# Kernel optimization log

Measured on AMD Instinct MI355X. Metric: run time of the kernel, lower is better.

## Reference

```python
import jax, jax.numpy as jnp
import numpy as np

C = 64
CK = C // 8  # query/key channels


def setup_inputs() -> dict:
    key = jax.random.key(0)
    ks = jax.random.split(key, 8)
    b, c, h, w = 4, C, 64, 64
    x = jax.random.normal(ks[0], (b, c, h, w), dtype=jnp.float32)
    # 1x1 conv weights (spectral-normalized weights are still just dense weights at eval)
    wq = jax.random.normal(ks[1], (CK, c), dtype=jnp.float32) * 0.05
    bq = jax.random.normal(ks[2], (CK,), dtype=jnp.float32) * 0.01
    wk = jax.random.normal(ks[3], (CK, c), dtype=jnp.float32) * 0.05
    bk = jax.random.normal(ks[4], (CK,), dtype=jnp.float32) * 0.01
    wv = jax.random.normal(ks[5], (c, c), dtype=jnp.float32) * 0.05
    bv = jax.random.normal(ks[6], (c,), dtype=jnp.float32) * 0.01
    # gamma is initialized to 0 in the module; use a nonzero value so the
    # attention path contributes to the output.
    gamma = jax.random.normal(ks[7], (1,), dtype=jnp.float32) * 0.5
    return {"x": x, "wq": wq, "bq": bq, "wk": wk, "bk": bk,
            "wv": wv, "bv": bv, "gamma": gamma}


def reference(x, wq, bq, wk, bk, wv, bv, gamma):
    b, c, h, w = x.shape
    n = h * w
    xf = x.reshape(b, c, n)                      # [b, c, n]
    # 1x1 convs as matmuls over the channel dim
    q = jnp.einsum('oc,bcn->bno', wq, xf) + bq   # [b, n, ck]
    k = jnp.einsum('oc,bcn->bon', wk, xf) + bk[None, :, None]  # [b, ck, n]
    v = jnp.einsum('oc,bcn->bno', wv, xf) + bv   # [b, n, c]
    attn = jax.nn.softmax(jnp.einsum('bnd,bdm->bnm', q, k), axis=-1)  # [b, n, n]
    o = jnp.einsum('bnm,bmc->bnc', attn, v)      # [b, n, c]
    o = o.transpose(0, 2, 1).reshape(b, c, h, w)
    return gamma[0] * o + x
```

## Files before the change

### kernel.cpp

```cpp
#include <hip/hip_runtime.h>

#define CH 64
#define NN 4096
#define NB 4
#define SPLIT 8
#define KLEN (NN / SPLIT)
#define KTILE 128
#define NT (KLEN / KTILE)
#define QBLK 256
#define LOG2E 1.44269504f

typedef unsigned short u16;
typedef unsigned int u32;
typedef __attribute__((ext_vector_type(8))) short bf16x8;
typedef __attribute__((ext_vector_type(16))) float f32x16;

static __device__ __forceinline__ u16 bf16r(float f) {
  union { float f; unsigned u; } v; v.f = f;
  unsigned x = v.u;
  x += 0x7fffu + ((x >> 16) & 1u);
  return (u16)(x >> 16);
}
static __device__ __forceinline__ u32 pk2(float a, float b) {
  union { float f; unsigned u; } va, vb; va.f = a; vb.f = b;
  unsigned x = va.u, y = vb.u;
  x += 0x7fffu + ((x >> 16) & 1u);
  y += 0x7fffu + ((y >> 16) & 1u);
  return (x >> 16) | (y & 0xffff0000u);
}

__global__ __launch_bounds__(128) void qkv_proj(
    const float* __restrict__ x,
    const float* __restrict__ wq, const float* __restrict__ bq,
    const float* __restrict__ wk, const float* __restrict__ bk,
    const float* __restrict__ wv, const float* __restrict__ bv,
    u16* __restrict__ Qb, u16* __restrict__ Kb, u16* __restrict__ Vb) {
  __shared__ u16 afr_lds[3][4][64][8];
  __shared__ float bvs[64];
  const int tid = threadIdx.x;

  for (int idx = tid; idx < 3 * 4 * 64; idx += 128) {
    const int l = idx & 63;
    const int s = (idx >> 6) & 3;
    const int t = idx >> 8;
    const int row = 32 * t + (l & 31);
    const int c0 = 16 * s + 8 * (l >> 5);
    float e[8];
#pragma unroll
    for (int j = 0; j < 8; ++j) {
      float v = 0.f;
      if (row < 64)      v = wv[row * 64 + c0 + j];
      else if (row < 72) v = wq[(row - 64) * 64 + c0 + j];
      else if (row < 80) v = wk[(row - 72) * 64 + c0 + j];
      e[j] = v;
    }
    u32* dst = reinterpret_cast<u32*>(&afr_lds[t][s][l][0]);
    dst[0] = pk2(e[0], e[1]); dst[1] = pk2(e[2], e[3]);
    dst[2] = pk2(e[4], e[5]); dst[3] = pk2(e[6], e[7]);
  }
  if (tid < 64) bvs[tid] = bv[tid];
  __syncthreads();

  const int b = blockIdx.x >> 6;
  const int n0 = (blockIdx.x & 63) << 6;
  const int w = tid >> 6;
  const int lane = tid & 63;
  const int l31 = lane & 31;
  const int h = lane >> 5;
  const int n = n0 + 32 * w + l31;

  bf16x8 afr[3][4];
#pragma unroll
  for (int t = 0; t < 3; ++t)
#pragma unroll
    for (int s = 0; s < 4; ++s)
      afr[t][s] = *reinterpret_cast<const bf16x8*>(&afr_lds[t][s][lane][0]);

  f32x16 acc[3] = {{}, {}, {}};
  const float* xb = x + (size_t)b * CH * NN + n;
#pragma unroll
  for (int s = 0; s < 4; ++s) {
    float xv[8];
#pragma unroll
    for (int j = 0; j < 8; ++j)
      xv[j] = xb[(size_t)(16 * s + 8 * h + j) * NN];
    union { uint4 u; bf16x8 v; } bf;
    bf.u.x = pk2(xv[0], xv[1]); bf.u.y = pk2(xv[2], xv[3]);
    bf.u.z = pk2(xv[4], xv[5]); bf.u.w = pk2(xv[6], xv[7]);
#pragma unroll
    for (int t = 0; t < 3; ++t)
      acc[t] = __builtin_amdgcn_mfma_f32_32x32x16_bf16(afr[t][s], bf.v, acc[t], 0, 0, 0);
  }

  const int sperm = (l31 & 19) | ((l31 & 4) << 1) | ((l31 & 8) >> 1);
  const int nperm = n0 + 32 * w + sperm;
#pragma unroll
  for (int t = 0; t < 2; ++t)
#pragma unroll
    for (int r = 0; r < 16; ++r) {
      const int row = 32 * t + (r & 3) + 8 * (r >> 2) + 4 * h;
      Vb[((size_t)b * CH + row) * NN + nperm] = bf16r(acc[t][r] + bvs[row]);
    }
#pragma unroll
  for (int r = 0; r < 8; ++r) {
    const int row = (r & 3) + 8 * (r >> 2) + 4 * h;
    const float v = acc[2][r];
    if (row < 8)
      Qb[((size_t)b * NN + n) * 8 + row] = bf16r((v + bq[row]) * LOG2E);
    else
      Kb[((size_t)b * NN + n) * 8 + (row - 8)] = bf16r(v + bk[row - 8]);
  }
}

__global__ __launch_bounds__(512, 4) void flash_attn(
    const u16* __restrict__ Qb, const u16* __restrict__ Kb,
    const u16* __restrict__ Vb, u32* __restrict__ ACCu,
    float* __restrict__ Lb) {
  __shared__ u16 Klds[2][1032];
  __shared__ u16 Vlds[2][8192];
  const int bid = blockIdx.x;
  const int sp = bid & 7;
  const int rest = bid >> 3;
  const int qb = rest & 15;
  const int b = rest >> 4;
  const int w = __builtin_amdgcn_readfirstlane(threadIdx.x >> 6);
  const int lane = threadIdx.x & 63;
  const int l31 = lane & 31;
  const int h = lane >> 5;
  const int x7 = l31 & 7;
  const int qrow0 = qb * QBLK + w * 32;
  const int ks = sp * KLEN;

  if (threadIdx.x < 8) {
    Klds[0][1024 + threadIdx.x] = 0;
    Klds[1][1024 + threadIdx.x] = 0;
  }

  bf16x8 qf = {0, 0, 0, 0, 0, 0, 0, 0};
  if (h == 0)
    qf = *reinterpret_cast<const bf16x8*>(Qb + ((size_t)b * NN + qrow0 + l31) * 8);

  const u16* Kp = Kb + ((size_t)b * NN + ks) * 8;
  const u16* Vp = Vb + (size_t)b * CH * NN + ks;

  const int c15 = lane & 15;
  const int vr0 = w * 8 + (lane >> 4);
  const int vr1 = vr0 + 4;
  const size_t vsrc0 = (size_t)vr0 * NN + (size_t)(((c15 & 8) | ((c15 ^ vr0) & 7)) * 8);
  const size_t vsrc1 = (size_t)vr1 * NN + (size_t)(((c15 & 8) | ((c15 ^ vr1) & 7)) * 8);

#define STAGE(tt, bb) do {                                                    \
    __builtin_amdgcn_global_load_lds(                                         \
        (const __attribute__((address_space(1))) void*)(Vp + vsrc0 + (tt) * KTILE), \
        (__attribute__((address_space(3))) void*)&Vlds[bb][(w * 8) * 128], 16, 0, 0); \
    __builtin_amdgcn_global_load_lds(                                         \
        (const __attribute__((address_space(1))) void*)(Vp + vsrc1 + (tt) * KTILE), \
        (__attribute__((address_space(3))) void*)&Vlds[bb][(w * 8 + 4) * 128], 16, 0, 0); \
    if (w < 2)                                                                \
      __builtin_amdgcn_global_load_lds(                                       \
          (const __attribute__((address_space(1))) void*)(Kp + ((size_t)(tt) * KTILE + w * 64 + lane) * 8), \
          (__attribute__((address_space(3))) void*)&Klds[bb][w * 512], 16, 0, 0); \
  } while (0)

  f32x16 acc0 = {}, acc1 = {};
  const f32x16 zz = {};
  float lsum = 0.f;

  STAGE(0, 0);
#pragma unroll
  for (int t = 0; t < NT; ++t) {
    const int buf = t & 1;
    __syncthreads();
    if (t + 1 < NT) STAGE(t + 1, buf ^ 1);
    const u16* Kl = &Klds[buf][0];
    const u16* Vl = &Vlds[buf][0];
#pragma unroll
    for (int k32 = 0; k32 < 4; ++k32) {
      const int kaddr = h ? 1024 : (k32 * 32 + l31) * 8;
      bf16x8 kf = *reinterpret_cast<const bf16x8*>(Kl + kaddr);
      f32x16 s = __builtin_amdgcn_mfma_f32_32x32x16_bf16(kf, qf, zz, 0, 0, 0);
      float p[16];
#pragma unroll
      for (int r = 0; r < 16; ++r) { p[r] = exp2f(s[r]); lsum += p[r]; }
      union { uint4 u; bf16x8 v; } pb0, pb1;
      pb0.u.x = pk2(p[0], p[1]);   pb0.u.y = pk2(p[2], p[3]);
      pb0.u.z = pk2(p[4], p[5]);   pb0.u.w = pk2(p[6], p[7]);
      pb1.u.x = pk2(p[8], p[9]);   pb1.u.y = pk2(p[10], p[11]);
      pb1.u.z = pk2(p[12], p[13]); pb1.u.w = pk2(p[14], p[15]);
      const int c16_0 = k32 * 4 + h;
      const int c16_1 = c16_0 + 2;
      const int cp0 = (c16_0 & 8) | ((c16_0 ^ x7) & 7);
      const int cp1 = (c16_1 & 8) | ((c16_1 ^ x7) & 7);
      bf16x8 v00 = *reinterpret_cast<const bf16x8*>(Vl + l31 * 128 + cp0 * 8);
      bf16x8 v01 = *reinterpret_cast<const bf16x8*>(Vl + l31 * 128 + cp1 * 8);
      bf16x8 v10 = *reinterpret_cast<const bf16x8*>(Vl + (32 + l31) * 128 + cp0 * 8);
      bf16x8 v11 = *reinterpret_cast<const bf16x8*>(Vl + (32 + l31) * 128 + cp1 * 8);
      acc0 = __builtin_amdgcn_mfma_f32_32x32x16_bf16(v00, pb0.v, acc0, 0, 0, 0);
      acc0 = __builtin_amdgcn_mfma_f32_32x32x16_bf16(v01, pb1.v, acc0, 0, 0, 0);
      acc1 = __builtin_amdgcn_mfma_f32_32x32x16_bf16(v10, pb0.v, acc1, 0, 0, 0);
      acc1 = __builtin_amdgcn_mfma_f32_32x32x16_bf16(v11, pb1.v, acc1, 0, 0, 0);
    }
  }
#undef STAGE

  lsum += __shfl_xor(lsum, 32);

  const int gtile = b * (NN / 32) + qb * 8 + w;
  u32* A = ACCu + ((size_t)gtile * SPLIT + sp) * 32 * 32;
#pragma unroll
  for (int rp = 0; rp < 8; ++rp) {
    const int chp = (rp & 1) + 4 * (rp >> 1) + 2 * h;
    __builtin_nontemporal_store(pk2(acc0[2 * rp], acc0[2 * rp + 1]),
                                &A[chp * 32 + l31]);
    __builtin_nontemporal_store(pk2(acc1[2 * rp], acc1[2 * rp + 1]),
                                &A[(16 + chp) * 32 + l31]);
  }
  if (h == 0)
    __builtin_nontemporal_store(lsum, &Lb[((size_t)gtile * SPLIT + sp) * 32 + l31]);
}

__global__ __launch_bounds__(256) void combine(
    const float* __restrict__ x, const float* __restrict__ gamma,
    const u32* __restrict__ ACCu, const float* __restrict__ Lb,
    float* __restrict__ out) {
  const int idx = blockIdx.x * 256 + threadIdx.x;
  const int n4 = idx & (NN / 4 - 1);
  const int cp = (idx >> 10) & 31;
  const int b = idx >> 15;
  const int n = n4 << 2;
  const int gtile = b * (NN / 32) + (n >> 5);
  const int q0 = n & 31;
  const uint4* A4 = reinterpret_cast<const uint4*>(ACCu);
  const float4* L4 = reinterpret_cast<const float4*>(Lb);
  float s0[4] = {0.f, 0.f, 0.f, 0.f}, s1[4] = {0.f, 0.f, 0.f, 0.f};
  float l[4] = {0.f, 0.f, 0.f, 0.f};
#pragma unroll
  for (int sp = 0; sp < SPLIT; ++sp) {
    const uint4 a = A4[(((size_t)gtile * SPLIT + sp) * 32 + cp) * 8 + (q0 >> 2)];
    const float4 lv = L4[(((size_t)gtile * SPLIT + sp) * 32 + q0) >> 2];
    const u32 av[4] = {a.x, a.y, a.z, a.w};
#pragma unroll
    for (int k = 0; k < 4; ++k) {
      union { u32 u; float f; } lo, hi;
      lo.u = av[k] << 16; hi.u = av[k] & 0xffff0000u;
      s0[k] += lo.f; s1[k] += hi.f;
    }
    l[0] += lv.x; l[1] += lv.y; l[2] += lv.z; l[3] += lv.w;
  }
  const float gm = gamma[0];
  float inv[4];
#pragma unroll
  for (int k = 0; k < 4; ++k) inv[k] = gm / l[k];
  const size_t i0 = ((size_t)b * CH + 2 * cp) * NN + n;
  const float4 x0 = *reinterpret_cast<const float4*>(x + i0);
  const float4 x1 = *reinterpret_cast<const float4*>(x + i0 + NN);
  float4 o0, o1;
  o0.x = fmaf(inv[0], s0[0], x0.x); o0.y = fmaf(inv[1], s0[1], x0.y);
  o0.z = fmaf(inv[2], s0[2], x0.z); o0.w = fmaf(inv[3], s0[3], x0.w);
  o1.x = fmaf(inv[0], s1[0], x1.x); o1.y = fmaf(inv[1], s1[1], x1.y);
  o1.z = fmaf(inv[2], s1[2], x1.z); o1.w = fmaf(inv[3], s1[3], x1.w);
  *reinterpret_cast<float4*>(out + i0) = o0;
  *reinterpret_cast<float4*>(out + i0 + NN) = o1;
}

extern "C" void kernel_launch(void* const* d_in, const int* in_sizes, int n_in,
                              void* d_out, int out_size, void* d_ws, size_t ws_size,
                              hipStream_t stream) {
  const float* x     = (const float*)d_in[0];
  const float* wq    = (const float*)d_in[1];
  const float* bq    = (const float*)d_in[2];
  const float* wk    = (const float*)d_in[3];
  const float* bk    = (const float*)d_in[4];
  const float* wv    = (const float*)d_in[5];
  const float* bv    = (const float*)d_in[6];
  const float* gamma = (const float*)d_in[7];
  float* out = (float*)d_out;

  u16* Qb = (u16*)d_ws;
  u16* Kb = Qb + (size_t)NB * NN * 8;
  u16* Vb = Kb + (size_t)NB * NN * 8;
  u32* ACCu = (u32*)(Vb + (size_t)NB * CH * NN);
  float* Lb = (float*)(ACCu + (size_t)NB * (NN / 32) * SPLIT * 32 * 32);

  qkv_proj<<<dim3(NB * (NN / 64)), dim3(128), 0, stream>>>(
      x, wq, bq, wk, bk, wv, bv, Qb, Kb, Vb);
  flash_attn<<<dim3(NB * (NN / QBLK) * SPLIT), dim3(512), 0, stream>>>(
      Qb, Kb, Vb, ACCu, Lb);
  combine<<<dim3((NB * 32 * (NN / 4)) / 256), dim3(256), 0, stream>>>(
      x, gamma, ACCu, Lb, out);
}
```

Baseline: 134.5 us.

## Load whole K/V split into LDS once and use 1024-thread attention blocks

The attention kernel now loads the entire 512-key K and V slice for its split into LDS up front with a padded, XOR-swizzled layout. It drops the double-buffered 128-key tile loop and per-tile barriers, and uses 16 waves of 512 queries per block to double K/V reuse. The projection kernel is restructured too: x is staged through LDS and each of three waves computes one output tile (V low, V high, Q/K), with 32 columns per block. The trade is more LDS per block, fewer blocks, and no overlap of loads with compute.

```diff
diff --git a/kernel.cpp b/kernel.cpp
--- a/kernel.cpp
+++ b/kernel.cpp
@@ -5,9 +5,7 @@
 #define NB 4
 #define SPLIT 8
 #define KLEN (NN / SPLIT)
-#define KTILE 128
-#define NT (KLEN / KTILE)
-#define QBLK 256
+#define VSTRIDE 520
 #define LOG2E 1.44269504f
 
 typedef unsigned short u16;
@@ -29,20 +27,24 @@
   return (x >> 16) | (y & 0xffff0000u);
 }
 
-__global__ __launch_bounds__(128) void qkv_proj(
+__global__ __launch_bounds__(192) void qkv_proj(
     const float* __restrict__ x,
     const float* __restrict__ wq, const float* __restrict__ bq,
     const float* __restrict__ wk, const float* __restrict__ bk,
     const float* __restrict__ wv, const float* __restrict__ bv,
     u16* __restrict__ Qb, u16* __restrict__ Kb, u16* __restrict__ Vb) {
+  __shared__ float xs[64 * 32];
   __shared__ u16 afr_lds[3][4][64][8];
-  __shared__ float bvs[64];
   const int tid = threadIdx.x;
-
-  for (int idx = tid; idx < 3 * 4 * 64; idx += 128) {
-    const int l = idx & 63;
-    const int s = (idx >> 6) & 3;
-    const int t = idx >> 8;
+  const int b = blockIdx.x >> 7;
+  const int n0 = (blockIdx.x & 127) << 5;
+
+  for (int i = tid; i < 64 * 32; i += 192)
+    xs[i] = x[(size_t)b * CH * NN + (size_t)(i >> 5) * NN + n0 + (i & 31)];
+  for (int i = tid; i < 768; i += 192) {
+    const int l = i & 63;
+    const int s = (i >> 6) & 3;
+    const int t = i >> 8;
     const int row = 32 * t + (l & 31);
     const int c0 = 16 * s + 8 * (l >> 5);
     float e[8];
@@ -58,83 +60,68 @@
     dst[0] = pk2(e[0], e[1]); dst[1] = pk2(e[2], e[3]);
     dst[2] = pk2(e[4], e[5]); dst[3] = pk2(e[6], e[7]);
   }
-  if (tid < 64) bvs[tid] = bv[tid];
   __syncthreads();
 
-  const int b = blockIdx.x >> 6;
-  const int n0 = (blockIdx.x & 63) << 6;
-  const int w = tid >> 6;
+  const int w = __builtin_amdgcn_readfirstlane(tid >> 6);
   const int lane = tid & 63;
   const int l31 = lane & 31;
   const int h = lane >> 5;
-  const int n = n0 + 32 * w + l31;
-
-  bf16x8 afr[3][4];
-#pragma unroll
-  for (int t = 0; t < 3; ++t)
-#pragma unroll
-    for (int s = 0; s < 4; ++s)
-      afr[t][s] = *reinterpret_cast<const bf16x8*>(&afr_lds[t][s][lane][0]);
-
-  f32x16 acc[3] = {{}, {}, {}};
-  const float* xb = x + (size_t)b * CH * NN + n;
+  const int n = n0 + l31;
+
+  f32x16 acc = {};
 #pragma unroll
   for (int s = 0; s < 4; ++s) {
     float xv[8];
 #pragma unroll
     for (int j = 0; j < 8; ++j)
-      xv[j] = xb[(size_t)(16 * s + 8 * h + j) * NN];
+      xv[j] = xs[(16 * s + 8 * h + j) * 32 + l31];
     union { uint4 u; bf16x8 v; } bf;
     bf.u.x = pk2(xv[0], xv[1]); bf.u.y = pk2(xv[2], xv[3]);
     bf.u.z = pk2(xv[4], xv[5]); bf.u.w = pk2(xv[6], xv[7]);
-#pragma unroll
-    for (int t = 0; t < 3; ++t)
-      acc[t] = __builtin_amdgcn_mfma_f32_32x32x16_bf16(afr[t][s], bf.v, acc[t], 0, 0, 0);
-  }
-
-  const int sperm = (l31 & 19) | ((l31 & 4) << 1) | ((l31 & 8) >> 1);
-  const int nperm = n0 + 32 * w + sperm;
-#pragma unroll
-  for (int t = 0; t < 2; ++t)
+    const bf16x8 af = *reinterpret_cast<const bf16x8*>(&afr_lds[w][s][lane][0]);
+    acc = __builtin_amdgcn_mfma_f32_32x32x16_bf16(af, bf.v, acc, 0, 0, 0);
+  }
+
+  if (w < 2) {
+    const int sperm = (l31 & 19) | ((l31 & 4) << 1) | ((l31 & 8) >> 1);
+    const int nperm = n0 + sperm;
 #pragma unroll
     for (int r = 0; r < 16; ++r) {
-      const int row = 32 * t + (r & 3) + 8 * (r >> 2) + 4 * h;
-      Vb[((size_t)b * CH + row) * NN + nperm] = bf16r(acc[t][r] + bvs[row]);
-    }
-#pragma unroll
-  for (int r = 0; r < 8; ++r) {
-    const int row = (r & 3) + 8 * (r >> 2) + 4 * h;
-    const float v = acc[2][r];
-    if (row < 8)
-      Qb[((size_t)b * NN + n) * 8 + row] = bf16r((v + bq[row]) * LOG2E);
-    else
-      Kb[((size_t)b * NN + n) * 8 + (row - 8)] = bf16r(v + bk[row - 8]);
-  }
-}
-
-__global__ __launch_bounds__(512, 4) void flash_attn(
+      const int row = 32 * w + (r & 3) + 8 * (r >> 2) + 4 * h;
+      Vb[((size_t)b * CH + row) * NN + nperm] = bf16r(acc[r] + bv[row]);
+    }
+  } else {
+#pragma unroll
+    for (int r = 0; r < 8; ++r) {
+      const int row = (r & 3) + 8 * (r >> 2) + 4 * h;
+      const float v = acc[r];
+      if (row < 8)
+        Qb[((size_t)b * NN + n) * 8 + row] = bf16r((v + bq[row]) * LOG2E);
+      else
+        Kb[((size_t)b * NN + n) * 8 + (row - 8)] = bf16r(v + bk[row - 8]);
+    }
+  }
+}
+
+__global__ __launch_bounds__(1024, 4) void flash_attn(
     const u16* __restrict__ Qb, const u16* __restrict__ Kb,
     const u16* __restrict__ Vb, u32* __restrict__ ACCu,
     float* __restrict__ Lb) {
-  __shared__ u16 Klds[2][1032];
-  __shared__ u16 Vlds[2][8192];
+  __shared__ u16 Klds[KLEN * 8 + 8];
+  __shared__ u16 Vlds[64 * VSTRIDE];
   const int bid = blockIdx.x;
   const int sp = bid & 7;
   const int rest = bid >> 3;
-  const int qb = rest & 15;
-  const int b = rest >> 4;
+  const int qc = rest & 7;
+  const int b = rest >> 3;
   const int w = __builtin_amdgcn_readfirstlane(threadIdx.x >> 6);
   const int lane = threadIdx.x & 63;
   const int l31 = lane & 31;
   const int h = lane >> 5;
-  const int x7 = l31 & 7;
-  const int qrow0 = qb * QBLK + w * 32;
+  const int qrow0 = qc * 512 + w * 32;
   const int ks = sp * KLEN;
 
-  if (threadIdx.x < 8) {
-    Klds[0][1024 + threadIdx.x] = 0;
-    Klds[1][1024 + threadIdx.x] = 0;
-  }
+  if (threadIdx.x < 8) Klds[KLEN * 8 + threadIdx.x] = 0;
 
   bf16x8 qf = {0, 0, 0, 0, 0, 0, 0, 0};
   if (h == 0)
@@ -143,69 +130,59 @@
   const u16* Kp = Kb + ((size_t)b * NN + ks) * 8;
   const u16* Vp = Vb + (size_t)b * CH * NN + ks;
 
-  const int c15 = lane & 15;
-  const int vr0 = w * 8 + (lane >> 4);
-  const int vr1 = vr0 + 4;
-  const size_t vsrc0 = (size_t)vr0 * NN + (size_t)(((c15 & 8) | ((c15 ^ vr0) & 7)) * 8);
-  const size_t vsrc1 = (size_t)vr1 * NN + (size_t)(((c15 & 8) | ((c15 ^ vr1) & 7)) * 8);
-
-#define STAGE(tt, bb) do {                                                    \
-    __builtin_amdgcn_global_load_lds(                                         \
-        (const __attribute__((address_space(1))) void*)(Vp + vsrc0 + (tt) * KTILE), \
-        (__attribute__((address_space(3))) void*)&Vlds[bb][(w * 8) * 128], 16, 0, 0); \
-    __builtin_amdgcn_global_load_lds(                                         \
-        (const __attribute__((address_space(1))) void*)(Vp + vsrc1 + (tt) * KTILE), \
-        (__attribute__((address_space(3))) void*)&Vlds[bb][(w * 8 + 4) * 128], 16, 0, 0); \
-    if (w < 2)                                                                \
-      __builtin_amdgcn_global_load_lds(                                       \
-          (const __attribute__((address_space(1))) void*)(Kp + ((size_t)(tt) * KTILE + w * 64 + lane) * 8), \
-          (__attribute__((address_space(3))) void*)&Klds[bb][w * 512], 16, 0, 0); \
-  } while (0)
+#pragma unroll
+  for (int i = 0; i < 4; ++i) {
+    const int ch = 4 * w + i;
+    const int m = (ch ^ (ch >> 3)) & 7;
+    const u16* src = Vp + (size_t)ch * NN + (((lane & 56) | ((lane ^ m) & 7)) << 3);
+    __builtin_amdgcn_global_load_lds(
+        (const __attribute__((address_space(1))) void*)src,
+        (__attribute__((address_space(3))) void*)&Vlds[ch * VSTRIDE], 16, 0, 0);
+  }
+  if (w < 8)
+    __builtin_amdgcn_global_load_lds(
+        (const __attribute__((address_space(1))) void*)(Kp + ((size_t)(64 * w + lane)) * 8),
+        (__attribute__((address_space(3))) void*)&Klds[64 * w * 8], 16, 0, 0);
+  __syncthreads();
 
   f32x16 acc0 = {}, acc1 = {};
   const f32x16 zz = {};
   float lsum = 0.f;
-
-  STAGE(0, 0);
-#pragma unroll
-  for (int t = 0; t < NT; ++t) {
-    const int buf = t & 1;
-    __syncthreads();
-    if (t + 1 < NT) STAGE(t + 1, buf ^ 1);
-    const u16* Kl = &Klds[buf][0];
-    const u16* Vl = &Vlds[buf][0];
-#pragma unroll
-    for (int k32 = 0; k32 < 4; ++k32) {
-      const int kaddr = h ? 1024 : (k32 * 32 + l31) * 8;
-      bf16x8 kf = *reinterpret_cast<const bf16x8*>(Kl + kaddr);
-      f32x16 s = __builtin_amdgcn_mfma_f32_32x32x16_bf16(kf, qf, zz, 0, 0, 0);
-      float p[16];
-#pragma unroll
-      for (int r = 0; r < 16; ++r) { p[r] = exp2f(s[r]); lsum += p[r]; }
-      union { uint4 u; bf16x8 v; } pb0, pb1;
-      pb0.u.x = pk2(p[0], p[1]);   pb0.u.y = pk2(p[2], p[3]);
-      pb0.u.z = pk2(p[4], p[5]);   pb0.u.w = pk2(p[6], p[7]);
-      pb1.u.x = pk2(p[8], p[9]);   pb1.u.y = pk2(p[10], p[11]);
-      pb1.u.z = pk2(p[12], p[13]); pb1.u.w = pk2(p[14], p[15]);
-      const int c16_0 = k32 * 4 + h;
-      const int c16_1 = c16_0 + 2;
-      const int cp0 = (c16_0 & 8) | ((c16_0 ^ x7) & 7);
-      const int cp1 = (c16_1 & 8) | ((c16_1 ^ x7) & 7);
-      bf16x8 v00 = *reinterpret_cast<const bf16x8*>(Vl + l31 * 128 + cp0 * 8);
-      bf16x8 v01 = *reinterpret_cast<const bf16x8*>(Vl + l31 * 128 + cp1 * 8);
-      bf16x8 v10 = *reinterpret_cast<const bf16x8*>(Vl + (32 + l31) * 128 + cp0 * 8);
-      bf16x8 v11 = *reinterpret_cast<const bf16x8*>(Vl + (32 + l31) * 128 + cp1 * 8);
-      acc0 = __builtin_amdgcn_mfma_f32_32x32x16_bf16(v00, pb0.v, acc0, 0, 0, 0);
-      acc0 = __builtin_amdgcn_mfma_f32_32x32x16_bf16(v01, pb1.v, acc0, 0, 0, 0);
-      acc1 = __builtin_amdgcn_mfma_f32_32x32x16_bf16(v10, pb0.v, acc1, 0, 0, 0);
-      acc1 = __builtin_amdgcn_mfma_f32_32x32x16_bf16(v11, pb1.v, acc1, 0, 0, 0);
-    }
-  }
-#undef STAGE
+  const int m0 = (l31 ^ (l31 >> 3)) & 7;
+  const int m1 = m0 ^ 4;
+
+#pragma unroll 4
+  for (int kk = 0; kk < KLEN / 32; ++kk) {
+    const int kaddr = h ? KLEN * 8 : (kk * 32 + l31) * 8;
+    bf16x8 kf = *reinterpret_cast<const bf16x8*>(Klds + kaddr);
+    f32x16 s = __builtin_amdgcn_mfma_f32_32x32x16_bf16(kf, qf, zz, 0, 0, 0);
+    float p[16];
+#pragma unroll
+    for (int r = 0; r < 16; ++r) { p[r] = exp2f(s[r]); lsum += p[r]; }
+    union { uint4 u; bf16x8 v; } pb0, pb1;
+    pb0.u.x = pk2(p[0], p[1]);   pb0.u.y = pk2(p[2], p[3]);
+    pb0.u.z = pk2(p[4], p[5]);   pb0.u.w = pk2(p[6], p[7]);
+    pb1.u.x = pk2(p[8], p[9]);   pb1.u.y = pk2(p[10], p[11]);
+    pb1.u.z = pk2(p[12], p[13]); pb1.u.w = pk2(p[14], p[15]);
+    const int g0 = kk * 4 + h;
+    const int g1 = g0 + 2;
+    const int cp00 = (g0 & 56) | ((g0 ^ m0) & 7);
+    const int cp01 = (g1 & 56) | ((g1 ^ m0) & 7);
+    const int cp10 = (g0 & 56) | ((g0 ^ m1) & 7);
+    const int cp11 = (g1 & 56) | ((g1 ^ m1) & 7);
+    bf16x8 v00 = *reinterpret_cast<const bf16x8*>(Vlds + l31 * VSTRIDE + cp00 * 8);
+    bf16x8 v01 = *reinterpret_cast<const bf16x8*>(Vlds + l31 * VSTRIDE + cp01 * 8);
+    bf16x8 v10 = *reinterpret_cast<const bf16x8*>(Vlds + (32 + l31) * VSTRIDE + cp10 * 8);
+    bf16x8 v11 = *reinterpret_cast<const bf16x8*>(Vlds + (32 + l31) * VSTRIDE + cp11 * 8);
+    acc0 = __builtin_amdgcn_mfma_f32_32x32x16_bf16(v00, pb0.v, acc0, 0, 0, 0);
+    acc0 = __builtin_amdgcn_mfma_f32_32x32x16_bf16(v01, pb1.v, acc0, 0, 0, 0);
+    acc1 = __builtin_amdgcn_mfma_f32_32x32x16_bf16(v10, pb0.v, acc1, 0, 0, 0);
+    acc1 = __builtin_amdgcn_mfma_f32_32x32x16_bf16(v11, pb1.v, acc1, 0, 0, 0);
+  }
 
   lsum += __shfl_xor(lsum, 32);
 
-  const int gtile = b * (NN / 32) + qb * 8 + w;
+  const int gtile = b * (NN / 32) + qc * 16 + w;
   u32* A = ACCu + ((size_t)gtile * SPLIT + sp) * 32 * 32;
 #pragma unroll
   for (int rp = 0; rp < 8; ++rp) {
@@ -282,9 +259,9 @@
   u32* ACCu = (u32*)(Vb + (size_t)NB * CH * NN);
   float* Lb = (float*)(ACCu + (size_t)NB * (NN / 32) * SPLIT * 32 * 32);
 
-  qkv_proj<<<dim3(NB * (NN / 64)), dim3(128), 0, stream>>>(
+  qkv_proj<<<dim3(NB * (NN / 32)), dim3(192), 0, stream>>>(
       x, wq, bq, wk, bk, wv, bv, Qb, Kb, Vb);
-  flash_attn<<<dim3(NB * (NN / QBLK) * SPLIT), dim3(512), 0, stream>>>(
+  flash_attn<<<dim3(NB * 8 * SPLIT), dim3(1024), 0, stream>>>(
       Qb, Kb, Vb, ACCu, Lb);
   combine<<<dim3((NB * 32 * (NN / 4)) / 256), dim3(256), 0, stream>>>(
       x, gamma, ACCu, Lb, out);
```

Measured after the change: 115.4 us. 14.2% less time.
